# Performance work log

Measured on AMD Instinct MI355X. Metric: run time of the kernel, lower is better.

## Reference

```python
import jax, jax.numpy as jnp
import numpy as np

B, S, D, V, T, NS, NG = 16, 512, 400, 32000, 8, 30, 3


def setup_inputs() -> dict:
    key = jax.random.key(0)
    ks = jax.random.split(key, 14)
    w = 1.0 / np.sqrt(D)
    return {
        "encoded_hidden": jax.random.normal(ks[0], (1, B, D), jnp.float32) * 0.1,
        "encoded_outputs": jax.random.normal(ks[1], (B, S, D), jnp.float32) * 0.1,
        "story": jax.random.randint(ks[2], (B, S), 0, V),
        "trg_batches": jax.random.randint(ks[3], (B, NS, T), 0, V),
        "shared_emb": jax.random.normal(ks[4], (V, D), jnp.float32) * 0.1,
        "slot_emb": jax.random.normal(ks[5], (1, D), jnp.float32) * 0.1,
        "w_ih": jax.random.normal(ks[6], (3 * D, D), jnp.float32) * w,
        "w_hh": jax.random.normal(ks[7], (3 * D, D), jnp.float32) * w,
        "b_ih": jax.random.normal(ks[8], (3 * D,), jnp.float32) * w,
        "b_hh": jax.random.normal(ks[9], (3 * D,), jnp.float32) * w,
        "w_ratio_w": jax.random.normal(ks[10], (1, 3 * D), jnp.float32) * w,
        "w_ratio_b": jax.random.normal(ks[11], (1,), jnp.float32) * w,
        "w_gate_w": jax.random.normal(ks[12], (NG, D), jnp.float32) * w,
        "w_gate_b": jax.random.normal(ks[13], (NG,), jnp.float32) * w,
        "batch_size": B,
        "max_resp_len": T,
    }


def reference(encoded_hidden, encoded_outputs, story, trg_batches, shared_emb,
              slot_emb, w_ih, w_hh, b_ih, b_hh, w_ratio_w, w_ratio_b,
              w_gate_w, w_gate_b, batch_size, max_resp_len):
    # Original torch code returns inside the slot loop -> only slot 0 is decoded.
    # h0 is re-used as GRU initial state at EVERY step (no carried hidden), and
    # teacher forcing makes each step's input known, so all T steps vectorize.
    h0 = encoded_hidden[0]                         # (B, D)
    Bq, Tq = batch_size, max_resp_len
    Vq = shared_emb.shape[0]

    # decoder inputs: step 0 = slot embedding, steps 1..T-1 = emb(trg[:,0,i-1])
    x0 = jnp.broadcast_to(slot_emb, h0.shape)      # (B, D)
    xt = shared_emb[trg_batches[:, 0, : Tq - 1]]   # (B, T-1, D)
    X = jnp.concatenate([x0[:, None, :], xt], axis=1)  # (B, T, D)

    # GRU cell (torch gate order r, z, n), h0 broadcast over steps
    gi = X @ w_ih.T + b_ih                         # (B, T, 3D)
    gh = h0 @ w_hh.T + b_hh                        # (B, 3D)
    i_r, i_z, i_n = jnp.split(gi, 3, axis=-1)
    h_r, h_z, h_n = jnp.split(gh, 3, axis=-1)
    r = jax.nn.sigmoid(i_r + h_r[:, None, :])
    z = jax.nn.sigmoid(i_z + h_z[:, None, :])
    n = jnp.tanh(i_n + r * h_n[:, None, :])
    h = (1.0 - z) * n + z * h0[:, None, :]         # (B, T, D) decoder_state == hidden

    # attention over history (no length masking: all lens == S)
    scores = jnp.einsum('btd,bsd->bts', h, encoded_outputs)   # (B, T, S)
    probs = jax.nn.softmax(scores, axis=-1)
    # FAITHFUL to original bug: context uses raw scores, not probs
    context = jnp.einsum('bts,bsd->btd', scores, encoded_outputs)

    gate0 = context[:, 0, :] @ w_gate_w.T + w_gate_b          # (B, NG), step i==0

    p_vocab = jax.nn.softmax(h @ shared_emb.T, axis=-1)       # (B, T, V)
    p_gen = jax.nn.sigmoid(
        jnp.concatenate([h, context, X], axis=-1) @ w_ratio_w.T + w_ratio_b
    )                                                         # (B, T, 1)

    # pointer distribution: scatter_add probs onto vocab ids of the story
    p_ctx = jnp.zeros((Bq, Tq, Vq), p_vocab.dtype).at[
        jnp.arange(Bq)[:, None, None],
        jnp.arange(Tq)[None, :, None],
        story[:, None, :],
    ].add(probs)

    p_final = p_gen * p_vocab + (1.0 - p_gen) * p_ctx         # (B, T, V)

    ptr_outputs = jnp.zeros((NS, Bq, Tq, Vq), p_final.dtype).at[0].set(p_final)
    gate_outputs = jnp.zeros((NS, Bq, NG), gate0.dtype).at[0].set(gate0)
    return ptr_outputs, gate_outputs
```

## Files before the change

### kernel.cpp

```cpp
#include <hip/hip_runtime.h>

#define Bq 16
#define Sq 512
#define Dq 400
#define Vq 32000
#define Tq 8
#define NSq 30
#define NGq 3
#define BTq (Bq*Tq)
#define SLICE 4096000
#define PTR_TOTAL (30ull*SLICE)
#define GATE_TOTAL (NSq*Bq*NGq)

#define NCOMPUTE 250
#define NZERO 1813
#define ZPER 16384

#define GCOMPUTE 64
#define PCTX_ZB 250

#define FBLK 8
#define FCH (Vq/FBLK)

__device__ inline float sigmoidf_(float x) { return 1.0f / (1.0f + __expf(-x)); }

__device__ inline unsigned bf16rne(float x) {
    unsigned u = __float_as_uint(x);
    return (u + 0x7FFFu + ((u >> 16) & 1u)) >> 16;
}

__device__ inline float blockReduceSum(float v, float* red) {
    int tid = threadIdx.x;
    #pragma unroll
    for (int o = 32; o > 0; o >>= 1) v += __shfl_down(v, o, 64);
    if ((tid & 63) == 0) red[tid >> 6] = v;
    __syncthreads();
    if (tid == 0) {
        float s = red[0];
        int nw = blockDim.x >> 6;
        for (int i = 1; i < nw; i++) s += red[i];
        red[0] = s;
    }
    __syncthreads();
    float r = red[0];
    __syncthreads();
    return r;
}

__device__ inline float blockReduceMax(float v, float* red) {
    int tid = threadIdx.x;
    #pragma unroll
    for (int o = 32; o > 0; o >>= 1) v = fmaxf(v, __shfl_down(v, o, 64));
    if ((tid & 63) == 0) red[tid >> 6] = v;
    __syncthreads();
    if (tid == 0) {
        float s = red[0];
        int nw = blockDim.x >> 6;
        for (int i = 1; i < nw; i++) s = fmaxf(s, red[i]);
        red[0] = s;
    }
    __syncthreads();
    float r = red[0];
    __syncthreads();
    return r;
}

__global__ __launch_bounds__(256) void k_gates(const float* __restrict__ enc_hidden,
                                               const float* __restrict__ shared_emb,
                                               const float* __restrict__ slot_emb,
                                               const float* __restrict__ w_ih,
                                               const float* __restrict__ w_hh,
                                               const float* __restrict__ b_ih,
                                               const float* __restrict__ b_hh,
                                               const int* __restrict__ trg,
                                               float* __restrict__ gi, float* __restrict__ gh,
                                               float* __restrict__ pctx) {
    int tid = threadIdx.x;
    if (blockIdx.x >= GCOMPUTE) {
        int zb = blockIdx.x - GCOMPUTE;
        float4 z = make_float4(0.0f, 0.0f, 0.0f, 0.0f);
        float4* dst = (float4*)pctx;
        size_t base = (size_t)zb * 4096 + tid;
        #pragma unroll
        for (int r = 0; r < 16; ++r) dst[base + (size_t)r * 256] = z;
        return;
    }
    __shared__ float A[9][Dq];
    __shared__ int toks[8];
    int b = blockIdx.x >> 2, jt = blockIdx.x & 3;
    if (tid < 7) toks[tid + 1] = trg[b * (NSq * Tq) + tid];
    __syncthreads();
    for (int idx = tid; idx < 900; idx += 256) {
        int r = idx / 100, q = idx - r * 100;
        const float4* src;
        if (r == 8)      src = (const float4*)(enc_hidden + b * Dq);
        else if (r == 0) src = (const float4*)slot_emb;
        else             src = (const float4*)(shared_emb + (size_t)toks[r] * Dq);
        *(float4*)&A[r][4 * q] = src[q];
    }
    __syncthreads();
    for (int o = tid; o < 2700; o += 256) {
        int r = o / 300, jj = o - r * 300;
        int j = jt * 300 + jj;
        const float* w = (r == 8) ? w_hh : w_ih;
        const float4* w4 = (const float4*)(w + (size_t)j * Dq);
        const float4* a4 = (const float4*)&A[r][0];
        float acc = (r == 8) ? b_hh[j] : b_ih[j];
        #pragma unroll 4
        for (int q = 0; q < Dq / 4; ++q) {
            float4 wv = w4[q], av = a4[q];
            acc += av.x * wv.x + av.y * wv.y + av.z * wv.z + av.w * wv.w;
        }
        if (r == 8) gh[b * 1200 + j] = acc;
        else        gi[(b * 8 + r) * 1200 + j] = acc;
    }
}

__global__ __launch_bounds__(512) void k_attn(const float* __restrict__ gi,
                                              const float* __restrict__ gh,
                                              const float* __restrict__ enc_hidden,
                                              const float* __restrict__ shared_emb,
                                              const float* __restrict__ slot_emb,
                                              const int* __restrict__ trg,
                                              const float* __restrict__ enc_out,
                                              const int* __restrict__ story,
                                              const float* __restrict__ w_ratio_w,
                                              const float* __restrict__ w_ratio_b,
                                              const float* __restrict__ w_gate_w,
                                              const float* __restrict__ w_gate_b,
                                              float* __restrict__ pctx, float* __restrict__ pgen,
                                              float* __restrict__ hT, float* __restrict__ out_gate) {
    __shared__ float h_l[Dq], ctx_l[Dq], x_l[Dq], sc_l[Sq], red[8];
    int bt = blockIdx.x, b = bt >> 3, t = bt & 7;
    int tid = threadIdx.x;
    if (tid < Dq) {
        int d = tid;
        float x = (t == 0) ? slot_emb[d]
                           : shared_emb[(size_t)trg[b * (NSq * Tq) + (t - 1)] * Dq + d];
        float h0 = enc_hidden[b * Dq + d];
        const float* gib = gi + bt * 1200;
        const float* ghb = gh + b * 1200;
        float r_ = sigmoidf_(gib[d] + ghb[d]);
        float z  = sigmoidf_(gib[Dq + d] + ghb[Dq + d]);
        float n  = tanhf(gib[2 * Dq + d] + r_ * ghb[2 * Dq + d]);
        float h  = (1.0f - z) * n + z * h0;
        h_l[d] = h; x_l[d] = x;
        hT[d * BTq + bt] = h;
    }
    __syncthreads();
    {
        const float4* e4 = (const float4*)(enc_out + ((size_t)(b * Sq + tid)) * Dq);
        float acc = 0.0f;
        for (int q = 0; q < Dq / 4; ++q) {
            float4 p = e4[q];
            int k = 4 * q;
            acc += h_l[k]*p.x + h_l[k+1]*p.y + h_l[k+2]*p.z + h_l[k+3]*p.w;
        }
        sc_l[tid] = acc;
    }
    __syncthreads();
    float myv = sc_l[tid];
    float m = blockReduceMax(myv, red);
    float e = __expf(myv - m);
    float ssum = blockReduceSum(e, red);
    atomicAdd(&pctx[(size_t)bt * Vq + story[b * Sq + tid]], e / ssum);
    for (int d = tid; d < Dq; d += 512) {
        float acc = 0.0f;
        #pragma unroll 8
        for (int s = 0; s < Sq; ++s)
            acc += sc_l[s] * enc_out[((size_t)(b * Sq + s)) * Dq + d];
        ctx_l[d] = acc;
    }
    __syncthreads();
    {
        float part = 0.0f;
        for (int i = tid; i < 1200; i += 512) {
            float v = (i < Dq) ? h_l[i] : (i < 2 * Dq ? ctx_l[i - Dq] : x_l[i - 2 * Dq]);
            part += v * w_ratio_w[i];
        }
        float tot = blockReduceSum(part, red);
        if (tid == 0) pgen[bt] = sigmoidf_(tot + w_ratio_b[0]);
    }
    if (t == 0) {
        for (int g = 0; g < NGq; ++g) {
            float part = 0.0f;
            for (int d = tid; d < Dq; d += 512) part += ctx_l[d] * w_gate_w[g * Dq + d];
            float tot = blockReduceSum(part, red);
            if (tid == 0) out_gate[b * NGq + g] = tot + w_gate_b[g];
        }
    }
}

#define TVL 128
#define CKL 40
__global__ __launch_bounds__(256) void k_logits(const float* __restrict__ hT,
                                                const float* __restrict__ emb,
                                                unsigned short* __restrict__ logits,
                                                float* __restrict__ pmax,
                                                float* __restrict__ psum,
                                                float* __restrict__ out) {
    __shared__ float eT[CKL][132];
    __shared__ float hL[CKL][132];
    int bid = blockIdx.x;
    int tid = threadIdx.x;
    if (bid >= NCOMPUTE) {
        int zb = bid - NCOMPUTE;
        float4 z = make_float4(0.0f, 0.0f, 0.0f, 0.0f);
        if (zb < NZERO) {
            float4* dst = (float4*)(out + (size_t)SLICE);
            const size_t total = 29ull * SLICE / 4;
            size_t base = (size_t)zb * ZPER + tid;
            #pragma unroll
            for (int r = 0; r < ZPER / 256; ++r) {
                size_t idx = base + (size_t)r * 256;
                if (idx < total) dst[idx] = z;
            }
        } else {
            float4* g = (float4*)(out + PTR_TOTAL + Bq * NGq);
            for (int i = tid; i < (GATE_TOTAL - Bq * NGq) / 4; i += 256) g[i] = z;
        }
        return;
    }
    int v0 = bid * TVL;
    int tx = tid & 15, ty = tid >> 4;
    float acc[8][8];
    #pragma unroll
    for (int j = 0; j < 8; ++j)
        #pragma unroll
        for (int i = 0; i < 8; ++i) acc[j][i] = 0.0f;

    for (int c = 0; c < Dq / CKL; ++c) {
        int k0 = c * CKL;
        const float4* hg = (const float4*)(hT + (size_t)k0 * BTq);
        #pragma unroll
        for (int r = 0; r < 5; ++r) {
            int idx = tid + 256 * r;
            int k = idx >> 5, c4 = idx & 31;
            float4 vd = hg[idx];
            *(float4*)&hL[k][4 * c4] = vd;
        }
        #pragma unroll
        for (int r = 0; r < 5; ++r) {
            int idx = tid + 256 * r;
            int v = idx / 10, q = idx - 10 * v;
            float4 vd = *(const float4*)(emb + (size_t)(v0 + v) * Dq + k0 + 4 * q);
            eT[4*q+0][v] = vd.x; eT[4*q+1][v] = vd.y; eT[4*q+2][v] = vd.z; eT[4*q+3][v] = vd.w;
        }
        __syncthreads();
        #pragma unroll 4
        for (int k = 0; k < CKL; ++k) {
            float4 h0 = *(const float4*)&hL[k][8 * ty];
            float4 h1 = *(const float4*)&hL[k][8 * ty + 4];
            float4 e0 = *(const float4*)&eT[k][8 * tx];
            float4 e1 = *(const float4*)&eT[k][8 * tx + 4];
            float hv[8] = {h0.x, h0.y, h0.z, h0.w, h1.x, h1.y, h1.z, h1.w};
            float ev[8] = {e0.x, e0.y, e0.z, e0.w, e1.x, e1.y, e1.z, e1.w};
            #pragma unroll
            for (int j = 0; j < 8; ++j)
                #pragma unroll
                for (int i = 0; i < 8; ++i)
                    acc[j][i] += hv[j] * ev[i];
        }
        __syncthreads();
    }
    #pragma unroll
    for (int j = 0; j < 8; ++j) {
        int bt = 8 * ty + j;
        unsigned bb[8];
        float r[8];
        float m = -1e30f;
        #pragma unroll
        for (int i = 0; i < 8; ++i) {
            bb[i] = bf16rne(acc[j][i]);
            r[i] = __uint_as_float(bb[i] << 16);
            m = fmaxf(m, r[i]);
        }
        #pragma unroll
        for (int o = 8; o >= 1; o >>= 1) m = fmaxf(m, __shfl_xor(m, o, 16));
        float es = 0.0f;
        #pragma unroll
        for (int i = 0; i < 8; ++i) es += __expf(r[i] - m);
        #pragma unroll
        for (int o = 8; o >= 1; o >>= 1) es += __shfl_xor(es, o, 16);
        if (tx == 0) {
            pmax[bid * BTq + bt] = m;
            psum[bid * BTq + bt] = es;
        }
        uint4 w = make_uint4(bb[0] | (bb[1] << 16), bb[2] | (bb[3] << 16),
                             bb[4] | (bb[5] << 16), bb[6] | (bb[7] << 16));
        *(uint4*)(logits + (size_t)bt * Vq + v0 + 8 * tx) = w;
    }
}

__global__ __launch_bounds__(256) void k_final(const unsigned short* __restrict__ logits,
                                               const float* __restrict__ pctx,
                                               const float* __restrict__ pgen,
                                               const float* __restrict__ pmax,
                                               const float* __restrict__ psum,
                                               float* __restrict__ out) {
    __shared__ float red[4];
    int bid = blockIdx.x, tid = threadIdx.x;
    int bt = bid >> 3, ch = bid & 7;
    float pm = (tid < NCOMPUTE) ? pmax[tid * BTq + bt] : -1e30f;
    float m = blockReduceMax(pm, red);
    float part = (tid < NCOMPUTE) ? psum[tid * BTq + bt] * __expf(pm - m) : 0.0f;
    float s = blockReduceSum(part, red);
    float inv = 1.0f / s, pg = pgen[bt], cg = 1.0f - pg;
    size_t rowoff = (size_t)bt * Vq + (size_t)ch * FCH;
    const uint4*  l4 = (const uint4*)(logits + rowoff);
    const float4* p4 = (const float4*)(pctx + rowoff);
    float4*       o4 = (float4*)(out + rowoff);
    for (int i = tid; i < FCH / 8; i += 256) {
        uint4 lv = l4[i];
        float4 pa = p4[2 * i], pb = p4[2 * i + 1];
        float f0 = __uint_as_float(lv.x << 16), f1 = __uint_as_float(lv.x & 0xFFFF0000u);
        float f2 = __uint_as_float(lv.y << 16), f3 = __uint_as_float(lv.y & 0xFFFF0000u);
        float f4 = __uint_as_float(lv.z << 16), f5 = __uint_as_float(lv.z & 0xFFFF0000u);
        float f6 = __uint_as_float(lv.w << 16), f7 = __uint_as_float(lv.w & 0xFFFF0000u);
        float4 oa = make_float4(pg * __expf(f0 - m) * inv + cg * pa.x,
                                pg * __expf(f1 - m) * inv + cg * pa.y,
                                pg * __expf(f2 - m) * inv + cg * pa.z,
                                pg * __expf(f3 - m) * inv + cg * pa.w);
        float4 ob = make_float4(pg * __expf(f4 - m) * inv + cg * pb.x,
                                pg * __expf(f5 - m) * inv + cg * pb.y,
                                pg * __expf(f6 - m) * inv + cg * pb.z,
                                pg * __expf(f7 - m) * inv + cg * pb.w);
        o4[2 * i]     = oa;
        o4[2 * i + 1] = ob;
    }
}

extern "C" void kernel_launch(void* const* d_in, const int* in_sizes, int n_in,
                              void* d_out, int out_size, void* d_ws, size_t ws_size,
                              hipStream_t stream) {
    const float* enc_hidden = (const float*)d_in[0];
    const float* enc_out    = (const float*)d_in[1];
    const int*   story      = (const int*)d_in[2];
    const int*   trg        = (const int*)d_in[3];
    const float* shared_emb = (const float*)d_in[4];
    const float* slot_emb   = (const float*)d_in[5];
    const float* w_ih       = (const float*)d_in[6];
    const float* w_hh       = (const float*)d_in[7];
    const float* b_ih       = (const float*)d_in[8];
    const float* b_hh       = (const float*)d_in[9];
    const float* w_ratio_w  = (const float*)d_in[10];
    const float* w_ratio_b  = (const float*)d_in[11];
    const float* w_gate_w   = (const float*)d_in[12];
    const float* w_gate_b   = (const float*)d_in[13];

    float* out = (float*)d_out;

    float* ws = (float*)d_ws;
    unsigned short* logits_buf = (unsigned short*)ws;
    float* pctx_buf   = ws + (size_t)SLICE;
    float* gi_buf     = ws + 2 * (size_t)SLICE;
    float* gh_buf     = gi_buf + 153600;
    float* hT_buf     = gh_buf + 19200;
    float* pgen_buf   = hT_buf + 51200;
    float* pmax_buf   = pgen_buf + 128;
    float* psum_buf   = pmax_buf + 32000;

    hipLaunchKernelGGL(k_gates, dim3(GCOMPUTE + PCTX_ZB), dim3(256), 0, stream,
                       enc_hidden, shared_emb, slot_emb, w_ih, w_hh, b_ih, b_hh, trg,
                       gi_buf, gh_buf, pctx_buf);
    hipLaunchKernelGGL(k_attn, dim3(BTq), dim3(512), 0, stream,
                       gi_buf, gh_buf, enc_hidden, shared_emb, slot_emb, trg,
                       enc_out, story, w_ratio_w, w_ratio_b, w_gate_w, w_gate_b,
                       pctx_buf, pgen_buf, hT_buf, out + PTR_TOTAL);
    hipLaunchKernelGGL(k_logits, dim3(NCOMPUTE + NZERO + 1), dim3(256), 0, stream,
                       hT_buf, shared_emb, logits_buf, pmax_buf, psum_buf, out);
    hipLaunchKernelGGL(k_final, dim3(BTq * FBLK), dim3(256), 0, stream,
                       logits_buf, pctx_buf, pgen_buf, pmax_buf, psum_buf, out);
}
```

Before: 750.7 us.

## Scatter pointer probs in shared memory and spread output zeroing across kernels

The dense p_ctx buffer (B*T*V floats) is dropped. k_attn now writes the compact softmax probs, and k_final scatter-adds them into a shared-memory chunk of the vocab row before writing that chunk out. This removes zero-filling, atomically updating and re-reading a 16 MB workspace buffer. Zeroing of the unused output slots is split across k_gates, k_attn and k_logits, so the tail work overlaps with compute blocks. Shared-memory atomics on colliding story tokens add some contention.

```diff
diff --git a/kernel.cpp b/kernel.cpp
--- a/kernel.cpp
+++ b/kernel.cpp
@@ -12,12 +12,14 @@
 #define PTR_TOTAL (30ull*SLICE)
 #define GATE_TOTAL (NSq*Bq*NGq)
 
+#define ZTOT 29696000ull
+#define ZPER 16384
+#define GZB 256
+#define AZB 384
+#define LZB 1173
+
 #define NCOMPUTE 250
-#define NZERO 1813
-#define ZPER 16384
-
 #define GCOMPUTE 64
-#define PCTX_ZB 250
 
 #define FBLK 8
 #define FCH (Vq/FBLK)
@@ -74,15 +76,18 @@
                                                const float* __restrict__ b_hh,
                                                const int* __restrict__ trg,
                                                float* __restrict__ gi, float* __restrict__ gh,
-                                               float* __restrict__ pctx) {
+                                               float* __restrict__ out) {
     int tid = threadIdx.x;
     if (blockIdx.x >= GCOMPUTE) {
         int zb = blockIdx.x - GCOMPUTE;
         float4 z = make_float4(0.0f, 0.0f, 0.0f, 0.0f);
-        float4* dst = (float4*)pctx;
-        size_t base = (size_t)zb * 4096 + tid;
-        #pragma unroll
-        for (int r = 0; r < 16; ++r) dst[base + (size_t)r * 256] = z;
+        float4* dst = (float4*)(out + (size_t)SLICE);
+        size_t base = (size_t)zb * ZPER + tid;
+        #pragma unroll
+        for (int r = 0; r < ZPER / 256; ++r) {
+            size_t idx = base + (size_t)r * 256;
+            if (idx < ZTOT) dst[idx] = z;
+        }
         return;
     }
     __shared__ float A[9][Dq];
@@ -128,11 +133,24 @@
                                               const float* __restrict__ w_ratio_b,
                                               const float* __restrict__ w_gate_w,
                                               const float* __restrict__ w_gate_b,
-                                              float* __restrict__ pctx, float* __restrict__ pgen,
-                                              float* __restrict__ hT, float* __restrict__ out_gate) {
+                                              float* __restrict__ probs, float* __restrict__ pgen,
+                                              float* __restrict__ hT, float* __restrict__ out_gate,
+                                              float* __restrict__ out) {
+    int tid = threadIdx.x;
+    if (blockIdx.x >= BTq) {
+        int zb = GZB + (blockIdx.x - BTq);
+        float4 z = make_float4(0.0f, 0.0f, 0.0f, 0.0f);
+        float4* dst = (float4*)(out + (size_t)SLICE);
+        size_t base = (size_t)zb * ZPER + tid;
+        #pragma unroll
+        for (int r = 0; r < ZPER / 512; ++r) {
+            size_t idx = base + (size_t)r * 512;
+            if (idx < ZTOT) dst[idx] = z;
+        }
+        return;
+    }
     __shared__ float h_l[Dq], ctx_l[Dq], x_l[Dq], sc_l[Sq], red[8];
     int bt = blockIdx.x, b = bt >> 3, t = bt & 7;
-    int tid = threadIdx.x;
     if (tid < Dq) {
         int d = tid;
         float x = (t == 0) ? slot_emb[d]
@@ -163,7 +181,7 @@
     float m = blockReduceMax(myv, red);
     float e = __expf(myv - m);
     float ssum = blockReduceSum(e, red);
-    atomicAdd(&pctx[(size_t)bt * Vq + story[b * Sq + tid]], e / ssum);
+    probs[bt * Sq + tid] = e / ssum;
     for (int d = tid; d < Dq; d += 512) {
         float acc = 0.0f;
         #pragma unroll 8
@@ -204,16 +222,16 @@
     int bid = blockIdx.x;
     int tid = threadIdx.x;
     if (bid >= NCOMPUTE) {
-        int zb = bid - NCOMPUTE;
+        int zl = bid - NCOMPUTE;
         float4 z = make_float4(0.0f, 0.0f, 0.0f, 0.0f);
-        if (zb < NZERO) {
+        if (zl < LZB) {
+            int zb = GZB + AZB + zl;
             float4* dst = (float4*)(out + (size_t)SLICE);
-            const size_t total = 29ull * SLICE / 4;
             size_t base = (size_t)zb * ZPER + tid;
             #pragma unroll
             for (int r = 0; r < ZPER / 256; ++r) {
                 size_t idx = base + (size_t)r * 256;
-                if (idx < total) dst[idx] = z;
+                if (idx < ZTOT) dst[idx] = z;
             }
         } else {
             float4* g = (float4*)(out + PTR_TOTAL + Bq * NGq);
@@ -293,41 +311,48 @@
 }
 
 __global__ __launch_bounds__(256) void k_final(const unsigned short* __restrict__ logits,
-                                               const float* __restrict__ pctx,
+                                               const float* __restrict__ probs,
+                                               const int* __restrict__ story,
                                                const float* __restrict__ pgen,
                                                const float* __restrict__ pmax,
                                                const float* __restrict__ psum,
                                                float* __restrict__ out) {
+    __shared__ float chunk[FCH];
     __shared__ float red[4];
     int bid = blockIdx.x, tid = threadIdx.x;
-    int bt = bid >> 3, ch = bid & 7;
+    int bt = bid >> 3, ch = bid & 7, b = bt >> 3;
     float pm = (tid < NCOMPUTE) ? pmax[tid * BTq + bt] : -1e30f;
     float m = blockReduceMax(pm, red);
     float part = (tid < NCOMPUTE) ? psum[tid * BTq + bt] * __expf(pm - m) : 0.0f;
     float s = blockReduceSum(part, red);
     float inv = 1.0f / s, pg = pgen[bt], cg = 1.0f - pg;
-    size_t rowoff = (size_t)bt * Vq + (size_t)ch * FCH;
-    const uint4*  l4 = (const uint4*)(logits + rowoff);
-    const float4* p4 = (const float4*)(pctx + rowoff);
-    float4*       o4 = (float4*)(out + rowoff);
+    int lo = ch * FCH;
+    const uint4* l4 = (const uint4*)(logits + (size_t)bt * Vq + lo);
     for (int i = tid; i < FCH / 8; i += 256) {
         uint4 lv = l4[i];
-        float4 pa = p4[2 * i], pb = p4[2 * i + 1];
         float f0 = __uint_as_float(lv.x << 16), f1 = __uint_as_float(lv.x & 0xFFFF0000u);
         float f2 = __uint_as_float(lv.y << 16), f3 = __uint_as_float(lv.y & 0xFFFF0000u);
         float f4 = __uint_as_float(lv.z << 16), f5 = __uint_as_float(lv.z & 0xFFFF0000u);
         float f6 = __uint_as_float(lv.w << 16), f7 = __uint_as_float(lv.w & 0xFFFF0000u);
-        float4 oa = make_float4(pg * __expf(f0 - m) * inv + cg * pa.x,
-                                pg * __expf(f1 - m) * inv + cg * pa.y,
-                                pg * __expf(f2 - m) * inv + cg * pa.z,
-                                pg * __expf(f3 - m) * inv + cg * pa.w);
-        float4 ob = make_float4(pg * __expf(f4 - m) * inv + cg * pb.x,
-                                pg * __expf(f5 - m) * inv + cg * pb.y,
-                                pg * __expf(f6 - m) * inv + cg * pb.z,
-                                pg * __expf(f7 - m) * inv + cg * pb.w);
-        o4[2 * i]     = oa;
-        o4[2 * i + 1] = ob;
-    }
+        chunk[8 * i + 0] = pg * __expf(f0 - m) * inv;
+        chunk[8 * i + 1] = pg * __expf(f1 - m) * inv;
+        chunk[8 * i + 2] = pg * __expf(f2 - m) * inv;
+        chunk[8 * i + 3] = pg * __expf(f3 - m) * inv;
+        chunk[8 * i + 4] = pg * __expf(f4 - m) * inv;
+        chunk[8 * i + 5] = pg * __expf(f5 - m) * inv;
+        chunk[8 * i + 6] = pg * __expf(f6 - m) * inv;
+        chunk[8 * i + 7] = pg * __expf(f7 - m) * inv;
+    }
+    __syncthreads();
+    for (int ss = tid; ss < Sq; ss += 256) {
+        int rel = story[b * Sq + ss] - lo;
+        if (rel >= 0 && rel < FCH)
+            atomicAdd(&chunk[rel], cg * probs[bt * Sq + ss]);
+    }
+    __syncthreads();
+    float4* o4 = (float4*)(out + (size_t)bt * Vq + lo);
+    const float4* c4 = (const float4*)chunk;
+    for (int i = tid; i < FCH / 4; i += 256) o4[i] = c4[i];
 }
 
 extern "C" void kernel_launch(void* const* d_in, const int* in_sizes, int n_in,
@@ -352,7 +377,7 @@
 
     float* ws = (float*)d_ws;
     unsigned short* logits_buf = (unsigned short*)ws;
-    float* pctx_buf   = ws + (size_t)SLICE;
+    float* probs_buf  = ws + (size_t)SLICE;
     float* gi_buf     = ws + 2 * (size_t)SLICE;
     float* gh_buf     = gi_buf + 153600;
     float* hT_buf     = gh_buf + 19200;
@@ -360,15 +385,15 @@
     float* pmax_buf   = pgen_buf + 128;
     float* psum_buf   = pmax_buf + 32000;
 
-    hipLaunchKernelGGL(k_gates, dim3(GCOMPUTE + PCTX_ZB), dim3(256), 0, stream,
+    hipLaunchKernelGGL(k_gates, dim3(GCOMPUTE + GZB), dim3(256), 0, stream,
                        enc_hidden, shared_emb, slot_emb, w_ih, w_hh, b_ih, b_hh, trg,
-                       gi_buf, gh_buf, pctx_buf);
-    hipLaunchKernelGGL(k_attn, dim3(BTq), dim3(512), 0, stream,
+                       gi_buf, gh_buf, out);
+    hipLaunchKernelGGL(k_attn, dim3(BTq + AZB), dim3(512), 0, stream,
                        gi_buf, gh_buf, enc_hidden, shared_emb, slot_emb, trg,
                        enc_out, story, w_ratio_w, w_ratio_b, w_gate_w, w_gate_b,
-                       pctx_buf, pgen_buf, hT_buf, out + PTR_TOTAL);
-    hipLaunchKernelGGL(k_logits, dim3(NCOMPUTE + NZERO + 1), dim3(256), 0, stream,
+                       probs_buf, pgen_buf, hT_buf, out + PTR_TOTAL, out);
+    hipLaunchKernelGGL(k_logits, dim3(NCOMPUTE + LZB + 1), dim3(256), 0, stream,
                        hT_buf, shared_emb, logits_buf, pmax_buf, psum_buf, out);
     hipLaunchKernelGGL(k_final, dim3(BTq * FBLK), dim3(256), 0, stream,
-                       logits_buf, pctx_buf, pgen_buf, pmax_buf, psum_buf, out);
-}
+                       logits_buf, probs_buf, story, pgen_buf, pmax_buf, psum_buf, out);
+}
```

New measurement: 742.6 us. No clear change (-1.1%).
